# Kernel tuning notes

Measured on AMD Instinct MI355X. Metric: run time of the kernel, lower is better.

The kernel has to match this reference:

```python
import jax, jax.numpy as jnp
import numpy as np

B, T, E, H = 2, 2048, 768, 12
DH = E // H  # per-head attention dim
EPS = 1e-5


def setup_inputs() -> dict:
    key = jax.random.key(0)
    ks = jax.random.split(key, 12)
    s = 0.02
    return {
        "x": jax.random.normal(ks[0], (B, T, E), dtype=jnp.float32),
        # stacked per-head projection weights: [H, E, DH], biases [H, DH]
        "Wq": jax.random.normal(ks[1], (H, E, DH), dtype=jnp.float32) * s,
        "bq": jax.random.normal(ks[2], (H, DH), dtype=jnp.float32) * s,
        "Wk": jax.random.normal(ks[3], (H, E, DH), dtype=jnp.float32) * s,
        "bk": jax.random.normal(ks[4], (H, DH), dtype=jnp.float32) * s,
        "Wv": jax.random.normal(ks[5], (H, E, DH), dtype=jnp.float32) * s,
        "bv": jax.random.normal(ks[6], (H, DH), dtype=jnp.float32) * s,
        "Wo": jax.random.normal(ks[7], (E, E), dtype=jnp.float32) * s,
        "bo": jax.random.normal(ks[8], (E,), dtype=jnp.float32) * s,
        "gamma": jnp.ones((E,), dtype=jnp.float32),
        "beta": jnp.zeros((E,), dtype=jnp.float32),
    }


def reference(x, Wq, bq, Wk, bk, Wv, bv, Wo, bo, gamma, beta):
    # per-head projections (heads stacked on axis h)
    q = jnp.einsum("bte,hed->bhtd", x, Wq) + bq[None, :, None, :]
    k = jnp.einsum("bte,hed->bhtd", x, Wk) + bk[None, :, None, :]
    v = jnp.einsum("bte,hed->bhtd", x, Wv) + bv[None, :, None, :]

    scores = jnp.einsum("bhtd,bhsd->bhts", q, k) / jnp.sqrt(jnp.float32(DH))
    causal = jnp.tril(jnp.ones((T, T), dtype=bool))  # True = keep
    scores = jnp.where(causal[None, None], scores, -jnp.inf)
    attn = jax.nn.softmax(scores, axis=-1)
    o = jnp.einsum("bhts,bhsd->bhtd", attn, v)  # [B,H,T,DH]

    # concat heads in head order -> [B,T,E]
    concat = jnp.transpose(o, (0, 2, 1, 3)).reshape(B, T, E)
    proj = concat @ Wo + bo

    # LayerNorm(proj) then residual add
    mu = jnp.mean(proj, axis=-1, keepdims=True)
    var = jnp.mean((proj - mu) ** 2, axis=-1, keepdims=True)
    normed = (proj - mu) * jax.lax.rsqrt(var + EPS) * gamma + beta
    return x + normed
```

## Files before the change

### kernel.cpp

```cpp
#include <hip/hip_runtime.h>
#include <stdint.h>

#define NROWS 4096
#define EMB   768
#define NQKV  2304
#define TSEQ  2048
#define NHEAD 12
#define NBH   24

typedef unsigned short u16;
typedef u16  ushort4v __attribute__((ext_vector_type(4)));
typedef u16  ushort8 __attribute__((ext_vector_type(8)));
typedef __bf16 bf16x8 __attribute__((ext_vector_type(8)));
typedef float f32x4 __attribute__((ext_vector_type(4)));

typedef const __attribute__((address_space(1))) void* gas_ptr;
typedef __attribute__((address_space(3))) void* las_ptr;

__device__ __forceinline__ u16 f2bf(float f) {
  union { float f; uint32_t u; } v; v.f = f;
  uint32_t u = v.u;
  return (u16)((u + 0x7fffu + ((u >> 16) & 1u)) >> 16);
}
__device__ __forceinline__ float bf2f(u16 u) {
  union { uint32_t u; float f; } v; v.u = ((uint32_t)u) << 16;
  return v.f;
}
__device__ __forceinline__ uint32_t cvtpk(float lo, float hi) {
  uint32_t r;
  asm("v_cvt_pk_bf16_f32 %0, %1, %2" : "=v"(r) : "v"(lo), "v"(hi));
  return r;
}

#define VMCNT0 asm volatile("s_waitcnt vmcnt(0)" ::: "memory")
#define LGKM0  asm volatile("s_waitcnt lgkmcnt(0)" ::: "memory")
#define SBAR   __builtin_amdgcn_s_barrier()
#define SCHED0 __builtin_amdgcn_sched_barrier(0)

__global__ __launch_bounds__(256) void k_pack(const float* __restrict__ x, u16* __restrict__ xb,
                                              const float* __restrict__ Wq, const float* __restrict__ Wk,
                                              const float* __restrict__ Wv, u16* __restrict__ wt,
                                              const float* __restrict__ Wo, u16* __restrict__ wot,
                                              uint32_t* __restrict__ cnt) {
  int bid = blockIdx.x, tid = threadIdx.x;
  if (bid == 0 && tid < 8) cnt[tid] = 0;
  if (bid < 1536) {
    int i = bid * 2048 + tid * 8;
    float4 a = *(const float4*)(x + i);
    float4 b = *(const float4*)(x + i + 4);
    uint4 o;
    o.x = cvtpk(a.x, a.y); o.y = cvtpk(a.z, a.w);
    o.z = cvtpk(b.x, b.y); o.w = cvtpk(b.z, b.w);
    *(uint4*)(xb + i) = o;
    return;
  }
  __shared__ u16 lds[64][68];
  if (bid < 1968) {
    int t = bid - 1536;
    int sel = t / 144, rest = t - sel * 144;
    int h = rest / 12, ec = rest - h * 12;
    const float* W = sel == 0 ? Wq : (sel == 1 ? Wk : Wv);
    const float* src = W + ((size_t)(h * EMB + ec * 64) * 64);
    int e = tid >> 2, d0 = (tid & 3) * 16;
#pragma unroll
    for (int j = 0; j < 4; ++j) {
      float4 v = *(const float4*)(src + (size_t)e * 64 + d0 + 4 * j);
      ushort4v pk;
      uint32_t w0 = cvtpk(v.x, v.y), w1 = cvtpk(v.z, v.w);
      pk[0] = (u16)(w0 & 0xffff); pk[1] = (u16)(w0 >> 16);
      pk[2] = (u16)(w1 & 0xffff); pk[3] = (u16)(w1 >> 16);
      *(ushort4v*)(&lds[e][d0 + 4 * j]) = pk;
    }
    __syncthreads();
    int d = tid >> 2, e0 = (tid & 3) * 16;
    ushort8 o0, o1;
#pragma unroll
    for (int j = 0; j < 8; ++j) { o0[j] = lds[e0 + j][d]; o1[j] = lds[e0 + 8 + j][d]; }
    int n = sel * EMB + h * 64 + d;
    u16* dst = wt + (size_t)n * EMB + ec * 64 + e0;
    *(ushort8*)dst = o0;
    *(ushort8*)(dst + 8) = o1;
  } else {
    int t = bid - 1968;
    int er = t / 12, nc = t - er * 12;
    int e = tid >> 2, n0 = (tid & 3) * 16;
#pragma unroll
    for (int j = 0; j < 4; ++j) {
      float4 v = *(const float4*)(Wo + (size_t)(er * 64 + e) * EMB + nc * 64 + n0 + 4 * j);
      ushort4v pk;
      uint32_t w0 = cvtpk(v.x, v.y), w1 = cvtpk(v.z, v.w);
      pk[0] = (u16)(w0 & 0xffff); pk[1] = (u16)(w0 >> 16);
      pk[2] = (u16)(w1 & 0xffff); pk[3] = (u16)(w1 >> 16);
      *(ushort4v*)(&lds[e][n0 + 4 * j]) = pk;
    }
    __syncthreads();
    int n = tid >> 2, e0 = (tid & 3) * 16;
    ushort8 o0, o1;
#pragma unroll
    for (int j = 0; j < 8; ++j) { o0[j] = lds[e0 + j][n]; o1[j] = lds[e0 + 8 + j][n]; }
    u16* dst = wot + (size_t)(nc * 64 + n) * EMB + er * 64 + e0;
    *(ushort8*)dst = o0;
    *(ushort8*)(dst + 8) = o1;
  }
}

template<int BM, int BN, int OUT_MODE>
__global__ __launch_bounds__(256) void k_gemm(const u16* __restrict__ A, const u16* __restrict__ Bt,
                                              const float* __restrict__ b0, const float* __restrict__ b1,
                                              const float* __restrict__ b2, void* __restrict__ Cout,
                                              u16* __restrict__ vtout, int M, int N, int K) {
  constexpr int MR = BM / 32, NR = BN / 32;
  __shared__ u16 lds_a[BM * 64];
  __shared__ u16 lds_b[BN * 64];
  int tid = threadIdx.x;
  int w = tid >> 6, lane = tid & 63;
  int wr = w >> 1, wc = w & 1;
  int m0 = blockIdx.x * BM, n0 = blockIdx.y * BN;
  int lrow = lane & 15, g = lane >> 4;

  f32x4 zero = {0.f, 0.f, 0.f, 0.f};
  f32x4 acc[MR][NR];
  for (int m = 0; m < MR; ++m) for (int n = 0; n < NR; ++n) acc[m][n] = zero;

  int l8 = lane >> 3, c8 = lane & 7;

  for (int k0 = 0; k0 < K; k0 += 64) {
#pragma unroll
    for (int i = 0; i < BM / 32; ++i) {
      int row = w * (BM / 4) + 8 * i + l8;
      int c16 = c8 ^ (row & 7);
      const u16* ga = A + (size_t)(m0 + row) * K + k0 + c16 * 8;
      __builtin_amdgcn_global_load_lds((gas_ptr)ga, (las_ptr)(lds_a + (w * (BM / 4) + 8 * i) * 64), 16, 0, 0);
    }
#pragma unroll
    for (int i = 0; i < BN / 32; ++i) {
      int row = w * (BN / 4) + 8 * i + l8;
      int c16 = c8 ^ (row & 7);
      const u16* gb = Bt + (size_t)(n0 + row) * K + k0 + c16 * 8;
      __builtin_amdgcn_global_load_lds((gas_ptr)gb, (las_ptr)(lds_b + (w * (BN / 4) + 8 * i) * 64), 16, 0, 0);
    }
    __syncthreads();
    bf16x8 af[MR][2], bfr[NR][2];
#pragma unroll
    for (int m = 0; m < MR; ++m)
#pragma unroll
      for (int kc = 0; kc < 2; ++kc) {
        int row = wr * (BM / 2) + m * 16 + lrow;
        int ch = (kc * 4 + g) ^ (row & 7);
        af[m][kc] = *(const bf16x8*)(lds_a + row * 64 + ch * 8);
      }
#pragma unroll
    for (int n = 0; n < NR; ++n)
#pragma unroll
      for (int kc = 0; kc < 2; ++kc) {
        int row = wc * (BN / 2) + n * 16 + lrow;
        int ch = (kc * 4 + g) ^ (row & 7);
        bfr[n][kc] = *(const bf16x8*)(lds_b + row * 64 + ch * 8);
      }
#pragma unroll
    for (int kc = 0; kc < 2; ++kc)
#pragma unroll
      for (int m = 0; m < MR; ++m)
#pragma unroll
        for (int n = 0; n < NR; ++n)
          acc[m][n] = __builtin_amdgcn_mfma_f32_16x16x32_bf16(af[m][kc], bfr[n][kc], acc[m][n], 0, 0, 0);
    __syncthreads();
  }

#pragma unroll
  for (int m = 0; m < MR; ++m)
#pragma unroll
    for (int n = 0; n < NR; ++n) {
      int col = n0 + wc * (BN / 2) + n * 16 + lrow;
      float bcol;
      if (OUT_MODE == 1) bcol = b0[col];
      else {
        int sel = col >= 1536 ? 2 : (col >= 768 ? 1 : 0);
        const float* bs = sel == 0 ? b0 : (sel == 1 ? b1 : b2);
        bcol = bs[col - sel * EMB];
      }
      int row0 = m0 + wr * (BM / 2) + m * 16 + 4 * g;
      if (OUT_MODE == 2 && col >= 2 * EMB) {
        int c = col - 2 * EMB;
        int hh = c >> 6, d = c & 63;
        int bb = row0 >> 11, t = row0 & 2047;
        int y = bb * NHEAD + hh;
        ushort4v pk;
#pragma unroll
        for (int r = 0; r < 4; ++r) pk[r] = f2bf(acc[m][n][r] + bcol);
        *(ushort4v*)(vtout + (size_t)(y * 64 + d) * TSEQ + t) = pk;
      } else {
#pragma unroll
        for (int r = 0; r < 4; ++r) {
          int row = row0 + r;
          float v = acc[m][n][r] + bcol;
          if (OUT_MODE == 1) ((float*)Cout)[(size_t)row * N + col] = v;
          else               ((u16*)Cout)[(size_t)row * N + col] = f2bf(v);
        }
      }
    }
}

__global__ __launch_bounds__(256, 3) void k_attn(const u16* __restrict__ qkv, const u16* __restrict__ vt,
                                                 u16* __restrict__ aout, uint32_t* __restrict__ cnt,
                                                 u16* __restrict__ pO, float* __restrict__ pL) {
  __shared__ u16 kbuf[2][64 * 64];
  __shared__ u16 vbuf[2][64 * 64];
  __shared__ u16 pbuf[4][16 * 64];
  __shared__ int task_s;
  int tid = threadIdx.x;
  int w = tid >> 6, lane = tid & 63;
  int ql = lane & 15, g = lane >> 4;
  int xcd = blockIdx.x & 7;
  const float sc2 = 0.18033688f;
  u16* pw = &pbuf[w][0];
  int swz = (ql & 7) << 3;
  int l8 = lane >> 3, c8 = lane & 7;

  for (;;) {
    if (tid == 0) task_s = (int)atomicAdd(&cnt[xcd], 1u);
    __syncthreads();
    int tau = task_s;
    __syncthreads();
    if (tau >= 144) break;

    int rank = tau / 3, yl = tau - rank * 3;
    int qb, t0, t1ex, cslot; bool direct;
    if (rank < 16)       { qb = 16 + rank; t0 = 0;  t1ex = 16;     cslot = 0; direct = false; }
    else if (!(rank & 1)){ int i = (rank - 16) >> 1; qb = 31 - i; t0 = 16; t1ex = qb + 1; cslot = 1; direct = false; }
    else                 { int i = (rank - 16) >> 1; qb = 15 - i; t0 = 0;  t1ex = qb + 1; cslot = 0; direct = true; }

    int y = xcd * 3 + yl;
    int b = y / NHEAD, h = y - b * NHEAD;
    int qrow0w = qb * 64 + w * 16;
    int qg = qrow0w + ql;

    const u16* qp = qkv + (size_t)(b * TSEQ + qg) * NQKV + h * 64;
    bf16x8 bq0 = *(const bf16x8*)(qp + g * 8);
    bf16x8 bq1 = *(const bf16x8*)(qp + 32 + g * 8);

    const u16* kst = qkv + (size_t)(b * TSEQ) * NQKV + EMB + h * 64;
    const u16* vst = vt + (size_t)y * 64 * TSEQ;

    f32x4 zero = {0.f, 0.f, 0.f, 0.f};
    f32x4 o[4]; for (int n = 0; n < 4; ++n) o[n] = zero;
    float lr = 0.f;

    auto STAGE = [&](int bi, int t_) {
#pragma unroll
      for (int i = 0; i < 2; ++i) {
        int row = i * 32 + 8 * w + l8;
        int c16 = c8 ^ (row & 7);
        const u16* gk = kst + (size_t)(t_ * 64 + row) * NQKV + c16 * 8;
        __builtin_amdgcn_global_load_lds((gas_ptr)gk, (las_ptr)(&kbuf[bi][(i * 32 + 8 * w) * 64]), 16, 0, 0);
        const u16* gv = vst + (size_t)row * TSEQ + t_ * 64 + c16 * 8;
        __builtin_amdgcn_global_load_lds((gas_ptr)gv, (las_ptr)(&vbuf[bi][(i * 32 + 8 * w) * 64]), 16, 0, 0);
      }
    };

    STAGE(t0 & 1, t0);
    for (int t = t0; t < t1ex; ++t) {
      int cur = t & 1;
      VMCNT0;
      SBAR;
      if (t + 1 < t1ex) STAGE(cur ^ 1, t + 1);

      const u16* kb = &kbuf[cur][0];
      const u16* vb = &vbuf[cur][0];
      int s0 = t * 64;

      f32x4 st[4];
#pragma unroll
      for (int sblk = 0; sblk < 4; ++sblk) {
        int row = sblk * 16 + ql;
        bf16x8 ka0 = *(const bf16x8*)(kb + ((row * 64 + 8 * g) ^ swz));
        bf16x8 ka1 = *(const bf16x8*)(kb + ((row * 64 + 32 + 8 * g) ^ swz));
        f32x4 acc = zero;
        acc = __builtin_amdgcn_mfma_f32_16x16x32_bf16(ka0, bq0, acc, 0, 0, 0);
        acc = __builtin_amdgcn_mfma_f32_16x16x32_bf16(ka1, bq1, acc, 0, 0, 0);
        st[sblk] = acc;
      }

      bool lastt = (t == qb);
      float e[4][4];
#pragma unroll
      for (int sblk = 0; sblk < 4; ++sblk)
#pragma unroll
        for (int r = 0; r < 4; ++r) {
          float vv = __builtin_fmaf(st[sblk][r], sc2, -2.0f);
          if (lastt) {
            int sg = s0 + sblk * 16 + 4 * g + r;
            if (sg > qg) vv = -1e30f;
          }
          float ee = __builtin_amdgcn_exp2f(vv);
          e[sblk][r] = ee;
          lr += ee;
        }

#pragma unroll
      for (int sblk = 0; sblk < 4; ++sblk) {
        uint2 dw;
        dw.x = cvtpk(e[sblk][0], e[sblk][1]);
        dw.y = cvtpk(e[sblk][2], e[sblk][3]);
        *(uint2*)(pw + ((ql * 64 + sblk * 16 + 4 * g) ^ swz)) = dw;
      }
      LGKM0; SCHED0;
      bf16x8 ap0 = *(const bf16x8*)(pw + ((ql * 64 + 8 * g) ^ swz));
      bf16x8 ap1 = *(const bf16x8*)(pw + ((ql * 64 + 32 + 8 * g) ^ swz));

#pragma unroll
      for (int n = 0; n < 4; ++n) {
        int row = n * 16 + ql;
        bf16x8 vb0 = *(const bf16x8*)(vb + ((row * 64 + 8 * g) ^ swz));
        bf16x8 vb1 = *(const bf16x8*)(vb + ((row * 64 + 32 + 8 * g) ^ swz));
        o[n] = __builtin_amdgcn_mfma_f32_16x16x32_bf16(ap0, vb0, o[n], 0, 0, 0);
        o[n] = __builtin_amdgcn_mfma_f32_16x16x32_bf16(ap1, vb1, o[n], 0, 0, 0);
      }
    }

    float lw = lr;
    lw += __shfl_xor(lw, 16);
    lw += __shfl_xor(lw, 32);

    if (direct) {
      float linv = 1.0f / lw;
      float li[4];
#pragma unroll
      for (int r = 0; r < 4; ++r) li[r] = __shfl(linv, 4 * g + r);
#pragma unroll
      for (int n = 0; n < 4; ++n)
#pragma unroll
        for (int r = 0; r < 4; ++r) {
          int q = qrow0w + 4 * g + r;
          aout[(size_t)(b * TSEQ + q) * EMB + h * 64 + n * 16 + ql] = f2bf(o[n][r] * li[r]);
        }
    } else {
      int blk = y * 16 + (qb - 16);
      u16* po = pO + ((size_t)blk * 2 + cslot) * 4096;
      float* pl = pL + ((size_t)blk * 2 + cslot) * 64;
      if (g == 0) pl[w * 16 + ql] = lw;
#pragma unroll
      for (int n = 0; n < 4; ++n)
#pragma unroll
        for (int r = 0; r < 4; ++r) {
          int qloc = w * 16 + 4 * g + r;
          po[qloc * 64 + n * 16 + ql] = f2bf(o[n][r]);
        }
    }
  }
}

__global__ __launch_bounds__(256) void k_combine(const u16* __restrict__ pO, const float* __restrict__ pL,
                                                 u16* __restrict__ aout) {
  int blk = blockIdx.x;
  int y = blk >> 4, qb = 16 + (blk & 15);
  int b = y / NHEAD, h = y - b * NHEAD;
  int tid = threadIdx.x;
  int row = tid >> 2, c0 = (tid & 3) * 16;
  const u16* p0 = pO + ((size_t)blk * 2) * 4096 + row * 64 + c0;
  const u16* p1 = p0 + 4096;
  float l = pL[blk * 128 + row] + pL[blk * 128 + 64 + row];
  float rinv = 1.0f / l;
  ushort8 a0 = *(const ushort8*)(p0);
  ushort8 a1 = *(const ushort8*)(p0 + 8);
  ushort8 b0 = *(const ushort8*)(p1);
  ushort8 b1 = *(const ushort8*)(p1 + 8);
  ushort8 o0, o1;
#pragma unroll
  for (int j = 0; j < 8; j += 2) {
    uint32_t w0 = cvtpk((bf2f(a0[j]) + bf2f(b0[j])) * rinv, (bf2f(a0[j+1]) + bf2f(b0[j+1])) * rinv);
    o0[j] = (u16)(w0 & 0xffff); o0[j+1] = (u16)(w0 >> 16);
    uint32_t w1 = cvtpk((bf2f(a1[j]) + bf2f(b1[j])) * rinv, (bf2f(a1[j+1]) + bf2f(b1[j+1])) * rinv);
    o1[j] = (u16)(w1 & 0xffff); o1[j+1] = (u16)(w1 >> 16);
  }
  u16* dst = aout + (size_t)(b * TSEQ + qb * 64 + row) * EMB + h * 64 + c0;
  *(ushort8*)dst = o0;
  *(ushort8*)(dst + 8) = o1;
}

__global__ __launch_bounds__(256) void k_ln_res(const float* __restrict__ proj, const float* __restrict__ x,
                                                const float* __restrict__ gamma, const float* __restrict__ beta,
                                                float* __restrict__ out) {
  __shared__ float smem[2][4];
  int row = blockIdx.x;
  const float* pr = proj + (size_t)row * EMB;
  const float* xr = x + (size_t)row * EMB;
  float* orow = out + (size_t)row * EMB;
  int tid = threadIdx.x;
  float v[3];
  float s = 0.f, s2 = 0.f;
#pragma unroll
  for (int i = 0; i < 3; ++i) { v[i] = pr[tid + 256 * i]; s += v[i]; s2 += v[i] * v[i]; }
#pragma unroll
  for (int m = 1; m < 64; m <<= 1) { s += __shfl_xor(s, m); s2 += __shfl_xor(s2, m); }
  int w = tid >> 6, lane = tid & 63;
  if (lane == 0) { smem[0][w] = s; smem[1][w] = s2; }
  __syncthreads();
  s  = smem[0][0] + smem[0][1] + smem[0][2] + smem[0][3];
  s2 = smem[1][0] + smem[1][1] + smem[1][2] + smem[1][3];
  float mu = s * (1.f / EMB);
  float var = s2 * (1.f / EMB) - mu * mu;
  float rstd = rsqrtf(var + 1e-5f);
#pragma unroll
  for (int i = 0; i < 3; ++i) {
    int c = tid + 256 * i;
    orow[c] = xr[c] + (v[i] - mu) * rstd * gamma[c] + beta[c];
  }
}

extern "C" void kernel_launch(void* const* d_in, const int* in_sizes, int n_in,
                              void* d_out, int out_size, void* d_ws, size_t ws_size,
                              hipStream_t stream) {
  const float* x     = (const float*)d_in[0];
  const float* Wq    = (const float*)d_in[1];
  const float* bq    = (const float*)d_in[2];
  const float* Wk    = (const float*)d_in[3];
  const float* bk    = (const float*)d_in[4];
  const float* Wv    = (const float*)d_in[5];
  const float* bv    = (const float*)d_in[6];
  const float* Wo    = (const float*)d_in[7];
  const float* bo    = (const float*)d_in[8];
  const float* gamma = (const float*)d_in[9];
  const float* beta  = (const float*)d_in[10];
  float* out = (float*)d_out;

  char* ws = (char*)d_ws;
  size_t off = 0;
  u16* xb    = (u16*)(ws + off); off += (size_t)NROWS * EMB * 2;
  u16* wqkvt = (u16*)(ws + off); off += (size_t)NQKV * EMB * 2;
  u16* wot   = (u16*)(ws + off); off += (size_t)EMB * EMB * 2;
  uint32_t* cnt = (uint32_t*)(ws + off); off += 64;
  u16* qkv   = (u16*)(ws + off); off += (size_t)NROWS * NQKV * 2;
  u16* vt    = (u16*)(ws + off); off += (size_t)NBH * 64 * TSEQ * 2;
  u16* aout  = (u16*)(ws + off); off += (size_t)NROWS * EMB * 2;
  u16* pO    = (u16*)(ws + off); off += (size_t)NBH * 16 * 2 * 4096 * 2;
  float* pL  = (float*)(ws + off); off += (size_t)NBH * 16 * 2 * 64 * 4;
  float* proj = (float*)qkv;

  k_pack<<<dim3(2112), 256, 0, stream>>>(x, xb, Wq, Wk, Wv, wqkvt, Wo, wot, cnt);
  k_gemm<128, 128, 2><<<dim3(NROWS / 128, NQKV / 128), 256, 0, stream>>>(xb, wqkvt, bq, bk, bv, qkv, vt, NROWS, NQKV, EMB);
  k_attn<<<dim3(768), 256, 0, stream>>>(qkv, vt, aout, cnt, pO, pL);
  k_combine<<<dim3(NBH * 16), 256, 0, stream>>>(pO, pL, aout);
  k_gemm<128, 64, 1><<<dim3(NROWS / 128, EMB / 64), 256, 0, stream>>>(aout, wot, bo, nullptr, nullptr, proj, nullptr, NROWS, EMB, EMB);
  k_ln_res<<<NROWS, 256, 0, stream>>>(proj, x, gamma, beta, out);
}
```

Before: 114.5 us.

## Split causal attention into 8-tile KV chunks with longest-first task table

Replaces the two-way KV split of the causal attention with chunks of up to 8 KV tiles per query block. The resulting 80 tasks per head are ordered longest-first through a table precomputed in the pack kernel. The combine kernel now sums up to four partial outputs, and the attention kernel drops K double-buffering so it can raise occupancy to 4 blocks per CU with more launched workgroups. This aims at better load balance and more parallelism, at the cost of extra partial writes and combine traffic. Prefetch of the next K tile now waits for an extra barrier after the QK MFMAs.

```diff
diff --git a/kernel.cpp b/kernel.cpp
--- a/kernel.cpp
+++ b/kernel.cpp
@@ -41,9 +41,34 @@
                                               const float* __restrict__ Wq, const float* __restrict__ Wk,
                                               const float* __restrict__ Wv, u16* __restrict__ wt,
                                               const float* __restrict__ Wo, u16* __restrict__ wot,
-                                              uint32_t* __restrict__ cnt) {
+                                              uint32_t* __restrict__ cnt, uint32_t* __restrict__ tbl) {
   int bid = blockIdx.x, tid = threadIdx.x;
-  if (bid == 0 && tid < 8) cnt[tid] = 0;
+  if (bid == 0) {
+    if (tid < 8) cnt[tid] = 0;
+    if (tid >= 64 && tid < 144) {
+      int p = tid - 64;
+      int myqb = 0, myc = 0, k = 0;
+      for (int qb = 0; qb < 32; ++qb) {
+        int nch = (qb + 8) >> 3;
+        for (int c = 0; c < nch; ++c) { if (k == p) { myqb = qb; myc = c; } ++k; }
+      }
+      int t0 = myc * 8;
+      int t1 = (myqb + 1 < t0 + 8) ? myqb + 1 : t0 + 8;
+      int mylen = t1 - t0, myid = myqb * 4 + myc;
+      int rank = 0;
+      for (int qb = 0; qb < 32; ++qb) {
+        int nch = (qb + 8) >> 3;
+        for (int c = 0; c < nch; ++c) {
+          int u0 = c * 8;
+          int u1 = (qb + 1 < u0 + 8) ? qb + 1 : u0 + 8;
+          int l = u1 - u0, id = qb * 4 + c;
+          if (l > mylen || (l == mylen && id < myid)) ++rank;
+        }
+      }
+      tbl[rank] = (uint32_t)myqb | ((uint32_t)t0 << 8) | ((uint32_t)t1 << 16)
+                | ((uint32_t)myc << 24) | (myqb <= 7 ? 0x80000000u : 0u);
+    }
+  }
   if (bid < 1536) {
     int i = bid * 2048 + tid * 8;
     float4 a = *(const float4*)(x + i);
@@ -201,10 +226,11 @@
     }
 }
 
-__global__ __launch_bounds__(256, 3) void k_attn(const u16* __restrict__ qkv, const u16* __restrict__ vt,
+__global__ __launch_bounds__(256, 4) void k_attn(const u16* __restrict__ qkv, const u16* __restrict__ vt,
                                                  u16* __restrict__ aout, uint32_t* __restrict__ cnt,
+                                                 const uint32_t* __restrict__ tbl,
                                                  u16* __restrict__ pO, float* __restrict__ pL) {
-  __shared__ u16 kbuf[2][64 * 64];
+  __shared__ u16 kbuf[64 * 64];
   __shared__ u16 vbuf[2][64 * 64];
   __shared__ u16 pbuf[4][16 * 64];
   __shared__ int task_s;
@@ -222,13 +248,12 @@
     __syncthreads();
     int tau = task_s;
     __syncthreads();
-    if (tau >= 144) break;
+    if (tau >= 240) break;
 
     int rank = tau / 3, yl = tau - rank * 3;
-    int qb, t0, t1ex, cslot; bool direct;
-    if (rank < 16)       { qb = 16 + rank; t0 = 0;  t1ex = 16;     cslot = 0; direct = false; }
-    else if (!(rank & 1)){ int i = (rank - 16) >> 1; qb = 31 - i; t0 = 16; t1ex = qb + 1; cslot = 1; direct = false; }
-    else                 { int i = (rank - 16) >> 1; qb = 15 - i; t0 = 0;  t1ex = qb + 1; cslot = 0; direct = true; }
+    uint32_t te = tbl[rank];
+    int qb = te & 0xff, t0 = (te >> 8) & 0xff, t1ex = (te >> 16) & 0xff, cslot = (te >> 24) & 0x7f;
+    bool direct = (te >> 31) != 0;
 
     int y = xcd * 3 + yl;
     int b = y / NHEAD, h = y - b * NHEAD;
@@ -246,42 +271,48 @@
     f32x4 o[4]; for (int n = 0; n < 4; ++n) o[n] = zero;
     float lr = 0.f;
 
-    auto STAGE = [&](int bi, int t_) {
+    auto STAGE_K = [&](int t_) {
 #pragma unroll
       for (int i = 0; i < 2; ++i) {
         int row = i * 32 + 8 * w + l8;
         int c16 = c8 ^ (row & 7);
         const u16* gk = kst + (size_t)(t_ * 64 + row) * NQKV + c16 * 8;
-        __builtin_amdgcn_global_load_lds((gas_ptr)gk, (las_ptr)(&kbuf[bi][(i * 32 + 8 * w) * 64]), 16, 0, 0);
+        __builtin_amdgcn_global_load_lds((gas_ptr)gk, (las_ptr)(&kbuf[(i * 32 + 8 * w) * 64]), 16, 0, 0);
+      }
+    };
+    auto STAGE_V = [&](int bi, int t_) {
+#pragma unroll
+      for (int i = 0; i < 2; ++i) {
+        int row = i * 32 + 8 * w + l8;
+        int c16 = c8 ^ (row & 7);
         const u16* gv = vst + (size_t)row * TSEQ + t_ * 64 + c16 * 8;
         __builtin_amdgcn_global_load_lds((gas_ptr)gv, (las_ptr)(&vbuf[bi][(i * 32 + 8 * w) * 64]), 16, 0, 0);
       }
     };
 
-    STAGE(t0 & 1, t0);
+    STAGE_K(t0);
+    STAGE_V(t0 & 1, t0);
     for (int t = t0; t < t1ex; ++t) {
-      int cur = t & 1;
       VMCNT0;
       SBAR;
-      if (t + 1 < t1ex) STAGE(cur ^ 1, t + 1);
-
-      const u16* kb = &kbuf[cur][0];
-      const u16* vb = &vbuf[cur][0];
-      int s0 = t * 64;
 
       f32x4 st[4];
 #pragma unroll
       for (int sblk = 0; sblk < 4; ++sblk) {
         int row = sblk * 16 + ql;
-        bf16x8 ka0 = *(const bf16x8*)(kb + ((row * 64 + 8 * g) ^ swz));
-        bf16x8 ka1 = *(const bf16x8*)(kb + ((row * 64 + 32 + 8 * g) ^ swz));
+        bf16x8 ka0 = *(const bf16x8*)(kbuf + ((row * 64 + 8 * g) ^ swz));
+        bf16x8 ka1 = *(const bf16x8*)(kbuf + ((row * 64 + 32 + 8 * g) ^ swz));
         f32x4 acc = zero;
         acc = __builtin_amdgcn_mfma_f32_16x16x32_bf16(ka0, bq0, acc, 0, 0, 0);
         acc = __builtin_amdgcn_mfma_f32_16x16x32_bf16(ka1, bq1, acc, 0, 0, 0);
         st[sblk] = acc;
       }
+      SCHED0;
+      SBAR;
+      if (t + 1 < t1ex) { STAGE_K(t + 1); STAGE_V((t + 1) & 1, t + 1); }
 
       bool lastt = (t == qb);
+      int s0 = t * 64;
       float e[4][4];
 #pragma unroll
       for (int sblk = 0; sblk < 4; ++sblk)
@@ -308,6 +339,7 @@
       bf16x8 ap0 = *(const bf16x8*)(pw + ((ql * 64 + 8 * g) ^ swz));
       bf16x8 ap1 = *(const bf16x8*)(pw + ((ql * 64 + 32 + 8 * g) ^ swz));
 
+      const u16* vb = &vbuf[t & 1][0];
 #pragma unroll
       for (int n = 0; n < 4; ++n) {
         int row = n * 16 + ql;
@@ -335,9 +367,9 @@
           aout[(size_t)(b * TSEQ + q) * EMB + h * 64 + n * 16 + ql] = f2bf(o[n][r] * li[r]);
         }
     } else {
-      int blk = y * 16 + (qb - 16);
-      u16* po = pO + ((size_t)blk * 2 + cslot) * 4096;
-      float* pl = pL + ((size_t)blk * 2 + cslot) * 64;
+      int blk2 = (y * 24 + (qb - 8)) * 4 + cslot;
+      u16* po = pO + (size_t)blk2 * 4096;
+      float* pl = pL + (size_t)blk2 * 64;
       if (g == 0) pl[w * 16 + ql] = lw;
 #pragma unroll
       for (int n = 0; n < 4; ++n)
@@ -353,25 +385,31 @@
 __global__ __launch_bounds__(256) void k_combine(const u16* __restrict__ pO, const float* __restrict__ pL,
                                                  u16* __restrict__ aout) {
   int blk = blockIdx.x;
-  int y = blk >> 4, qb = 16 + (blk & 15);
+  int y = blk / 24, q8 = blk - y * 24, qb = q8 + 8;
+  int nch = (qb + 8) >> 3;
   int b = y / NHEAD, h = y - b * NHEAD;
   int tid = threadIdx.x;
   int row = tid >> 2, c0 = (tid & 3) * 16;
-  const u16* p0 = pO + ((size_t)blk * 2) * 4096 + row * 64 + c0;
-  const u16* p1 = p0 + 4096;
-  float l = pL[blk * 128 + row] + pL[blk * 128 + 64 + row];
+  float l = 0.f;
+  for (int c = 0; c < nch; ++c) l += pL[((size_t)blk * 4 + c) * 64 + row];
   float rinv = 1.0f / l;
-  ushort8 a0 = *(const ushort8*)(p0);
-  ushort8 a1 = *(const ushort8*)(p0 + 8);
-  ushort8 b0 = *(const ushort8*)(p1);
-  ushort8 b1 = *(const ushort8*)(p1 + 8);
+  float acc[16];
+#pragma unroll
+  for (int j = 0; j < 16; ++j) acc[j] = 0.f;
+  for (int c = 0; c < nch; ++c) {
+    const u16* p = pO + ((size_t)blk * 4 + c) * 4096 + row * 64 + c0;
+    ushort8 a0 = *(const ushort8*)p;
+    ushort8 a1 = *(const ushort8*)(p + 8);
+#pragma unroll
+    for (int j = 0; j < 8; ++j) { acc[j] += bf2f(a0[j]); acc[8 + j] += bf2f(a1[j]); }
+  }
   ushort8 o0, o1;
 #pragma unroll
   for (int j = 0; j < 8; j += 2) {
-    uint32_t w0 = cvtpk((bf2f(a0[j]) + bf2f(b0[j])) * rinv, (bf2f(a0[j+1]) + bf2f(b0[j+1])) * rinv);
-    o0[j] = (u16)(w0 & 0xffff); o0[j+1] = (u16)(w0 >> 16);
-    uint32_t w1 = cvtpk((bf2f(a1[j]) + bf2f(b1[j])) * rinv, (bf2f(a1[j+1]) + bf2f(b1[j+1])) * rinv);
-    o1[j] = (u16)(w1 & 0xffff); o1[j+1] = (u16)(w1 >> 16);
+    uint32_t w0 = cvtpk(acc[j] * rinv, acc[j + 1] * rinv);
+    o0[j] = (u16)(w0 & 0xffff); o0[j + 1] = (u16)(w0 >> 16);
+    uint32_t w1 = cvtpk(acc[8 + j] * rinv, acc[9 + j] * rinv);
+    o1[j] = (u16)(w1 & 0xffff); o1[j + 1] = (u16)(w1 >> 16);
   }
   u16* dst = aout + (size_t)(b * TSEQ + qb * 64 + row) * EMB + h * 64 + c0;
   *(ushort8*)dst = o0;
@@ -430,17 +468,18 @@
   u16* wqkvt = (u16*)(ws + off); off += (size_t)NQKV * EMB * 2;
   u16* wot   = (u16*)(ws + off); off += (size_t)EMB * EMB * 2;
   uint32_t* cnt = (uint32_t*)(ws + off); off += 64;
+  uint32_t* tbl = (uint32_t*)(ws + off); off += 512;
   u16* qkv   = (u16*)(ws + off); off += (size_t)NROWS * NQKV * 2;
   u16* vt    = (u16*)(ws + off); off += (size_t)NBH * 64 * TSEQ * 2;
   u16* aout  = (u16*)(ws + off); off += (size_t)NROWS * EMB * 2;
-  u16* pO    = (u16*)(ws + off); off += (size_t)NBH * 16 * 2 * 4096 * 2;
-  float* pL  = (float*)(ws + off); off += (size_t)NBH * 16 * 2 * 64 * 4;
+  u16* pO    = (u16*)(ws + off); off += (size_t)NBH * 24 * 4 * 4096 * 2;
+  float* pL  = (float*)(ws + off); off += (size_t)NBH * 24 * 4 * 64 * 4;
   float* proj = (float*)qkv;
 
-  k_pack<<<dim3(2112), 256, 0, stream>>>(x, xb, Wq, Wk, Wv, wqkvt, Wo, wot, cnt);
+  k_pack<<<dim3(2112), 256, 0, stream>>>(x, xb, Wq, Wk, Wv, wqkvt, Wo, wot, cnt, tbl);
   k_gemm<128, 128, 2><<<dim3(NROWS / 128, NQKV / 128), 256, 0, stream>>>(xb, wqkvt, bq, bk, bv, qkv, vt, NROWS, NQKV, EMB);
-  k_attn<<<dim3(768), 256, 0, stream>>>(qkv, vt, aout, cnt, pO, pL);
-  k_combine<<<dim3(NBH * 16), 256, 0, stream>>>(pO, pL, aout);
+  k_attn<<<dim3(1024), 256, 0, stream>>>(qkv, vt, aout, cnt, tbl, pO, pL);
+  k_combine<<<dim3(NBH * 24), 256, 0, stream>>>(pO, pL, aout);
   k_gemm<128, 64, 1><<<dim3(NROWS / 128, EMB / 64), 256, 0, stream>>>(aout, wot, bo, nullptr, nullptr, proj, nullptr, NROWS, EMB, EMB);
   k_ln_res<<<NROWS, 256, 0, stream>>>(proj, x, gamma, beta, out);
 }
```

New measurement: 123.1 us. +7.5%, slower.
